# Performance work log

Hardware: AMD Instinct MI355X
Metric: run time of the kernel (lower is better)

Reference implementation:

```python
import jax, jax.numpy as jnp
import numpy as np

B, S, D, H = 2, 2048, 1024, 16
DH = D // H
EPS = 1e-5
LAMBDA_INIT = 0.8


def setup_inputs() -> dict:
    key = jax.random.key(0)
    ks = jax.random.split(key, 16)
    w_std = 1.0 / np.sqrt(D)
    lam_std = LAMBDA_INIT / np.sqrt(DH)
    return {
        "x": jax.random.normal(ks[0], (B, S, D), jnp.float32),
        # Linear weights stored [in, out] (y = x @ W + b), equivalent to torch W.T
        "Wq": jax.random.normal(ks[1], (D, D), jnp.float32) * w_std,
        "bq": jax.random.normal(ks[2], (D,), jnp.float32) * 0.02,
        "Wk": jax.random.normal(ks[3], (D, D), jnp.float32) * w_std,
        "bk": jax.random.normal(ks[4], (D,), jnp.float32) * 0.02,
        "Wv": jax.random.normal(ks[5], (D, D), jnp.float32) * w_std,
        "bv": jax.random.normal(ks[6], (D,), jnp.float32) * 0.02,
        "Wo": jax.random.normal(ks[7], (D, D), jnp.float32) * w_std,
        "bo": jax.random.normal(ks[8], (D,), jnp.float32) * 0.02,
        "lq1": jax.random.normal(ks[9], (H, DH), jnp.float32) * lam_std,
        "lk1": jax.random.normal(ks[10], (H, DH), jnp.float32) * lam_std,
        "lq2": jax.random.normal(ks[11], (H, DH), jnp.float32) * lam_std,
        "lk2": jax.random.normal(ks[12], (H, DH), jnp.float32) * lam_std,
        # per-head GroupNorm(1, head_dim) affine params (torch default init)
        "gn_w": jnp.ones((H, DH), jnp.float32),
        "gn_b": jnp.zeros((H, DH), jnp.float32),
    }


def reference(x, Wq, bq, Wk, bk, Wv, bv, Wo, bo, lq1, lk1, lq2, lk2, gn_w, gn_b):
    b, s, d = x.shape
    h, dh = lq1.shape
    scale = dh ** -0.5

    q = (x @ Wq + bq).reshape(b, s, h, dh)
    k = (x @ Wk + bk).reshape(b, s, h, dh)
    v = (x @ Wv + bv).reshape(b, s, h, dh)

    # differential lambda per head: exp(<lq1,lk1>) - exp(<lq2,lk2>) + lambda_init
    lam = jnp.exp((lq1 * lk1).sum(-1)) - jnp.exp((lq2 * lk2).sum(-1)) + LAMBDA_INIT  # [H]

    scores = jnp.einsum("bihd,bjhd->bhij", q, k) * scale * lam[None, :, None, None]
    attn = jax.nn.softmax(scores, axis=-1)  # no mask in default call path
    out = jnp.einsum("bhij,bjhd->bihd", attn, v)  # [B,S,H,DH]

    # per-head GroupNorm(1, head_dim): normalize over (seq, head_dim) per (batch, head)
    mean = out.mean(axis=(1, 3), keepdims=True)
    var = out.var(axis=(1, 3), keepdims=True)
    normed = (out - mean) * jax.lax.rsqrt(var + EPS)
    normed = normed * gn_w[None, None, :, :] + gn_b[None, None, :, :]

    y = normed.reshape(b, s, d) @ Wo + bo
    return y
```

## Files before the change

### kernel.cpp

```cpp
#include <hip/hip_runtime.h>

#define S_LEN 2048
#define D_DIM 1024
#define H_NUM 16
#define DH 64
#define EPS_GN 1e-5f
#define LAMBDA_INIT 0.8f

typedef unsigned short bfu;
typedef __attribute__((ext_vector_type(8))) short bf16x8;
typedef __attribute__((ext_vector_type(4))) float f32x4;

union FragU { uint4 u; bf16x8 f; };

__device__ inline float bf2f(bfu u){
  union { unsigned int i; float f; } c; c.i = ((unsigned int)u) << 16; return c.f;
}
__device__ inline bfu f2bf(float f){
  union { float f; unsigned int u; } c; c.f = f;
  unsigned int r = c.u + 0x7fffu + ((c.u >> 16) & 1u);
  return (bfu)(r >> 16);
}
__device__ inline unsigned cvtpk(float lo, float hi){
  unsigned r;
  asm("v_cvt_pk_bf16_f32 %0, %1, %2" : "=v"(r) : "v"(lo), "v"(hi));
  return r;
}
__device__ inline void gload16(const void* g, void* lds){
  __builtin_amdgcn_global_load_lds(
      (const __attribute__((address_space(1))) void*)g,
      (__attribute__((address_space(3))) void*)lds, 16, 0, 0);
}
__device__ inline float ldx(const void* p, size_t i, int isf32){
  return isf32 ? ((const float*)p)[i] : bf2f(((const bfu*)p)[i]);
}
__device__ inline float wave_sum(float x){
  #pragma unroll
  for (int off = 32; off; off >>= 1) x += __shfl_xor(x, off, 64);
  return x;
}

__global__ void lambda_kernel(const void* __restrict__ lq1, const void* __restrict__ lk1,
                              const void* __restrict__ lq2, const void* __restrict__ lk2,
                              const unsigned int* __restrict__ gnw_bits,
                              int* __restrict__ flag, float* __restrict__ lam,
                              float* __restrict__ sums){
  const int isf32 = (gnw_bits[0] == 0x3F800000u) ? 1 : 0;
  int t = threadIdx.x;
  if (t == 0) flag[0] = isf32;
  sums[t] = 0.f;
  if (t < H_NUM){
    float s1 = 0.f, s2 = 0.f;
    for (int d = 0; d < DH; ++d){
      s1 += ldx(lq1, t*DH+d, isf32) * ldx(lk1, t*DH+d, isf32);
      s2 += ldx(lq2, t*DH+d, isf32) * ldx(lk2, t*DH+d, isf32);
    }
    lam[t] = expf(s1) - expf(s2) + LAMBDA_INIT;
  }
}

__global__ __launch_bounds__(256) void prep_all(
    const void* __restrict__ x,
    const void* __restrict__ w0, const void* __restrict__ w1,
    const void* __restrict__ w2, const void* __restrict__ w3,
    const int* __restrict__ flag, bfu* __restrict__ xb, bfu* __restrict__ wt)
{
  const int isf32 = flag[0];
  if (blockIdx.x < 2048){
    size_t i = ((size_t)blockIdx.x * 256 + threadIdx.x) * 8;
    if (isf32){
      const float* xf = (const float*)x;
      float4 a = *(const float4*)(xf + i);
      float4 b = *(const float4*)(xf + i + 4);
      bfu o[8] = {f2bf(a.x),f2bf(a.y),f2bf(a.z),f2bf(a.w),f2bf(b.x),f2bf(b.y),f2bf(b.z),f2bf(b.w)};
      *(uint4*)(xb + i) = *(const uint4*)o;
    } else {
      *(uint4*)(xb + i) = *(const uint4*)((const bfu*)x + i);
    }
    return;
  }
  const int widx = blockIdx.x - 2048;
  const int wsel = widx >> 8, tile = widx & 255;
  const void* W = (wsel==0)?w0:(wsel==1)?w1:(wsel==2)?w2:w3;
  bfu* dst = wt + (size_t)wsel * D_DIM * D_DIM;
  __shared__ float Ts[64][65];
  const int r0 = (tile >> 4) * 64, c0 = (tile & 15) * 64;
  const int ty = threadIdx.x >> 6, tx = threadIdx.x & 63;
  #pragma unroll
  for (int rr = 0; rr < 16; ++rr){
    int row = ty*16 + rr;
    Ts[row][tx] = ldx(W, (size_t)(r0 + row) * D_DIM + c0 + tx, isf32);
  }
  __syncthreads();
  #pragma unroll
  for (int rr = 0; rr < 16; ++rr){
    int row = ty*16 + rr;
    dst[(size_t)(c0 + row) * D_DIM + r0 + tx] = f2bf(Ts[tx][row]);
  }
}

__global__ __launch_bounds__(256, 3) void qkv_mfma(
    const bfu* __restrict__ xb, const bfu* __restrict__ wt,
    const void* __restrict__ bq, const void* __restrict__ bk, const void* __restrict__ bv,
    const float* __restrict__ lam, const int* __restrict__ flag,
    bfu* __restrict__ qb, bfu* __restrict__ kb, bfu* __restrict__ vt)
{
  const int isf32 = flag[0];
  const int z = blockIdx.z;
  const bfu* Wt = wt + (size_t)z * D_DIM * D_DIM;
  const void* bias = (z==0)?bq:(z==1)?bk:bv;

  __shared__ __align__(16) ushort As[2][128][32];
  __shared__ __align__(16) ushort Bs[2][128][32];
  const int m0 = blockIdx.x * 128, n0 = blockIdx.y * 128;
  const int t = threadIdx.x, w = t >> 6, lane = t & 63;
  const int quad = lane >> 4, l15 = lane & 15;
  const int mbase = (w >> 1) * 64, nbase = (w & 1) * 64;

  const int srow = w*32 + (lane >> 2);
  const int gchunk = (lane & 3) ^ ((lane >> 3) & 3);
  const size_t aoff = (size_t)(m0 + srow) * D_DIM + gchunk*8;
  const size_t boff = (size_t)(n0 + srow) * D_DIM + gchunk*8;

#define STAGE(buf, k0) {                                                  \
    gload16(xb + aoff + (k0),            &As[buf][w*32][0]);              \
    gload16(xb + aoff + 16*D_DIM + (k0), &As[buf][w*32+16][0]);           \
    gload16(Wt + boff + (k0),            &Bs[buf][w*32][0]);              \
    gload16(Wt + boff + 16*D_DIM + (k0), &Bs[buf][w*32+16][0]);           \
  }

  f32x4 acc[4][4];
  #pragma unroll
  for (int i = 0; i < 4; ++i)
    #pragma unroll
    for (int j = 0; j < 4; ++j){ f32x4 zz = {0.f,0.f,0.f,0.f}; acc[i][j] = zz; }

  const int chq = (quad ^ ((l15 >> 1) & 3)) * 8;

  STAGE(0, 0)
  int buf = 0;
  for (int k0 = 0; k0 < D_DIM; k0 += 32){
    if (k0 + 32 < D_DIM){
      STAGE(buf ^ 1, k0 + 32)
      asm volatile("s_waitcnt vmcnt(4)" ::: "memory");
    } else {
      asm volatile("s_waitcnt vmcnt(0)" ::: "memory");
    }
    __builtin_amdgcn_s_barrier();
    FragU af[4], bf[4];
    #pragma unroll
    for (int mt = 0; mt < 4; ++mt) af[mt].u = *(const uint4*)&As[buf][mbase + mt*16 + l15][chq];
    #pragma unroll
    for (int nt = 0; nt < 4; ++nt) bf[nt].u = *(const uint4*)&Bs[buf][nbase + nt*16 + l15][chq];
    #pragma unroll
    for (int mt = 0; mt < 4; ++mt)
      #pragma unroll
      for (int nt = 0; nt < 4; ++nt)
        acc[mt][nt] = __builtin_amdgcn_mfma_f32_16x16x32_bf16(af[mt].f, bf[nt].f, acc[mt][nt], 0, 0, 0);
    __builtin_amdgcn_s_barrier();
    buf ^= 1;
  }
#undef STAGE

  #pragma unroll
  for (int mt = 0; mt < 4; ++mt){
    const int mrow = m0 + mbase + mt*16 + quad*4;
    #pragma unroll
    for (int nt = 0; nt < 4; ++nt){
      const int n = n0 + nbase + nt*16 + l15;
      const float bn = ldx(bias, n, isf32);
      if (z < 2){
        bfu* out = (z == 0) ? qb : kb;
        const float qs = (z == 0) ? 0.18033688f * lam[n >> 6] : 1.0f;
        #pragma unroll
        for (int r = 0; r < 4; ++r)
          out[(size_t)(mrow + r) * D_DIM + n] = f2bf((acc[mt][nt][r] + bn) * qs);
      } else {
        const int b = mrow >> 11, s = mrow & (S_LEN - 1);
        const int h = n >> 6, d = n & 63;
        ushort4 pk;
        pk.x = f2bf(acc[mt][nt][0] + bn); pk.y = f2bf(acc[mt][nt][1] + bn);
        pk.z = f2bf(acc[mt][nt][2] + bn); pk.w = f2bf(acc[mt][nt][3] + bn);
        *(ushort4*)(vt + (((size_t)(b*H_NUM + h)*DH + d)*S_LEN) + s) = pk;
      }
    }
  }
}

__global__ __launch_bounds__(256) void repack_k(const bfu* __restrict__ kb, bfu* __restrict__ ksw){
  __shared__ __align__(16) ushort L[64][72];
  const int b = blockIdx.z, h = blockIdx.y, j0 = blockIdx.x * 64;
  const int t = threadIdx.x;
  const int bh = b*H_NUM + h;
  {
    const int j = t >> 2, seg = (t & 3) * 16;
    const bfu* src = kb + ((size_t)(b*S_LEN + j0 + j)*H_NUM + h)*DH + seg;
    uint4 a = *(const uint4*)src, c = *(const uint4*)(src + 8);
    *(uint4*)&L[j][seg] = a; *(uint4*)&L[j][seg+8] = c;
  }
  __syncthreads();
  #pragma unroll
  for (int half = 0; half < 2; ++half){
    int c16 = half*256 + t;
    int blk = c16 >> 6;
    int l   = c16 & 63;
    int jt = blk >> 1, c = blk & 1;
    int m = l & 15, q = l >> 4;
    uint4 v = *(const uint4*)&L[jt*16 + m][c*32 + q*8];
    bfu* dst = ksw + (((size_t)bh*128 + (j0>>4) + jt)*2 + c)*512 + (size_t)l*8;
    *(uint4*)dst = v;
  }
}

__global__ __launch_bounds__(256) void repack_v(const bfu* __restrict__ vt, bfu* __restrict__ vsw){
  __shared__ __align__(16) ushort L[64][72];
  const int b = blockIdx.z, h = blockIdx.y, j0 = blockIdx.x * 64;
  const int t = threadIdx.x;
  const int bh = b*H_NUM + h;
  {
    const int d = t >> 2, seg = (t & 3) * 16;
    const bfu* src = vt + ((size_t)bh*DH + d)*S_LEN + j0 + seg;
    uint4 a = *(const uint4*)src, c = *(const uint4*)(src + 8);
    *(uint4*)&L[d][seg] = a; *(uint4*)&L[d][seg+8] = c;
  }
  __syncthreads();
  #pragma unroll
  for (int half = 0; half < 2; ++half){
    int c16 = half*256 + t;
    int blk = c16 >> 6;
    int l   = c16 & 63;
    int dt = blk >> 1, jcl = blk & 1;
    int m = l & 15, q = l >> 4;
    const int jb = jcl*32 + 16*(q>>1) + 4*(q&1);
    uint2 v0 = *(const uint2*)&L[dt*16 + m][jb];
    uint2 v1 = *(const uint2*)&L[dt*16 + m][jb + 8];
    uint4 v; v.x = v0.x; v.y = v0.y; v.z = v1.x; v.w = v1.y;
    bfu* dst = vsw + (((size_t)bh*4 + dt)*64 + (j0>>5) + jcl)*512 + (size_t)l*8;
    *(uint4*)dst = v;
  }
}

__global__ __launch_bounds__(256, 2) void attn_mfma(
    const bfu* __restrict__ qb, const bfu* __restrict__ ksw, const bfu* __restrict__ vsw,
    bfu* __restrict__ o, float* __restrict__ sums)
{
  const int wg = blockIdx.x;
  const int swz = (wg & 7) * 64 + (wg >> 3);
  const int g = swz >> 4;
  const int i0 = (swz & 15) * 128;
  const int h = g & 15, b = g >> 4;
  const int t = threadIdx.x, w = t >> 6, lane = t & 63;
  const int quad = lane >> 4, l15 = lane & 15;
  const int bh = g;

  FragU qf[2][2];
  #pragma unroll
  for (int mt = 0; mt < 2; ++mt){
    const bfu* qrow = qb + ((size_t)(b*S_LEN + i0 + w*32 + mt*16 + l15)*H_NUM + h)*DH;
    qf[mt][0].u = *(const uint4*)(qrow + quad*8);
    qf[mt][1].u = *(const uint4*)(qrow + 32 + quad*8);
  }

  const bfu* kbase = ksw + (size_t)bh*131072 + (size_t)lane*8;
  const bfu* vbase = vsw + (size_t)bh*131072 + (size_t)lane*8;

  f32x4 Oacc[2][4];
  #pragma unroll
  for (int mt = 0; mt < 2; ++mt)
    #pragma unroll
    for (int dt = 0; dt < 4; ++dt){ f32x4 zz = {0.f,0.f,0.f,0.f}; Oacc[mt][dt] = zz; }
  float lsum[2] = {0.f, 0.f};

  FragU kfA[4][2], vfA[2][4], kfB[4][2], vfB[2][4];

#define LOAD_K(KF, J0)                                                          \
  { _Pragma("unroll")                                                           \
    for (int jt = 0; jt < 4; ++jt){                                             \
      const bfu* kr = kbase + (size_t)(((J0)>>4) + jt)*1024;                    \
      KF[jt][0].u = *(const uint4*)kr;                                          \
      KF[jt][1].u = *(const uint4*)(kr + 512);                                  \
    } }
#define LOAD_V(VF, J0)                                                          \
  { _Pragma("unroll")                                                           \
    for (int jt2 = 0; jt2 < 2; ++jt2)                                           \
      _Pragma("unroll")                                                         \
      for (int dt = 0; dt < 4; ++dt)                                            \
        VF[jt2][dt].u = *(const uint4*)(vbase + (size_t)(dt*64 + ((J0)>>5) + jt2)*512); }

#define PROCESS(KF, VF)                                                         \
  {                                                                             \
    f32x4 s[2][4];                                                              \
    __builtin_amdgcn_s_setprio(1);                                              \
    _Pragma("unroll")                                                           \
    for (int jt = 0; jt < 4; ++jt){                                             \
      _Pragma("unroll")                                                         \
      for (int mt = 0; mt < 2; ++mt){                                           \
        f32x4 zz = {0.f,0.f,0.f,0.f};                                           \
        zz = __builtin_amdgcn_mfma_f32_16x16x32_bf16(KF[jt][0].f, qf[mt][0].f, zz, 0, 0, 0); \
        zz = __builtin_amdgcn_mfma_f32_16x16x32_bf16(KF[jt][1].f, qf[mt][1].f, zz, 0, 0, 0); \
        s[mt][jt] = zz;                                                         \
      }                                                                         \
    }                                                                           \
    __builtin_amdgcn_s_setprio(0);                                              \
    _Pragma("unroll")                                                           \
    for (int mt = 0; mt < 2; ++mt){                                             \
      float ps = 0.f;                                                           \
      _Pragma("unroll")                                                         \
      for (int jt = 0; jt < 4; ++jt){                                           \
        _Pragma("unroll")                                                       \
        for (int r = 0; r < 4; ++r){                                            \
          float p = __builtin_exp2f(s[mt][jt][r]);                              \
          s[mt][jt][r] = p;                                                     \
          ps += p;                                                              \
        }                                                                       \
      }                                                                         \
      lsum[mt] += ps;                                                           \
      _Pragma("unroll")                                                         \
      for (int jt2 = 0; jt2 < 2; ++jt2){                                        \
        unsigned pa0 = cvtpk(s[mt][2*jt2][0],   s[mt][2*jt2][1]);               \
        unsigned pa1 = cvtpk(s[mt][2*jt2][2],   s[mt][2*jt2][3]);               \
        unsigned pb0 = cvtpk(s[mt][2*jt2+1][0], s[mt][2*jt2+1][1]);             \
        unsigned pb1 = cvtpk(s[mt][2*jt2+1][2], s[mt][2*jt2+1][3]);             \
        auto r0 = __builtin_amdgcn_permlane32_swap(pa0, pb0, false, false);     \
        auto r1 = __builtin_amdgcn_permlane32_swap(pa1, pb1, false, false);     \
        FragU pf;                                                               \
        pf.u.x = r0[0]; pf.u.y = r1[0]; pf.u.z = r0[1]; pf.u.w = r1[1];         \
        __builtin_amdgcn_s_setprio(1);                                          \
        _Pragma("unroll")                                                       \
        for (int dt = 0; dt < 4; ++dt)                                          \
          Oacc[mt][dt] = __builtin_amdgcn_mfma_f32_16x16x32_bf16(VF[jt2][dt].f, pf.f, Oacc[mt][dt], 0, 0, 0); \
        __builtin_amdgcn_s_setprio(0);                                          \
      }                                                                         \
    }                                                                           \
  }

  LOAD_K(kfA, 0)
  LOAD_V(vfA, 0)
  for (int j0 = 0; j0 < S_LEN; j0 += 128){
    LOAD_K(kfB, j0 + 64)
    LOAD_V(vfB, j0 + 64)
    PROCESS(kfA, vfA)
    if (j0 + 128 < S_LEN){
      LOAD_K(kfA, j0 + 128)
      LOAD_V(vfA, j0 + 128)
    }
    PROCESS(kfB, vfB)
  }
#undef LOAD_K
#undef LOAD_V
#undef PROCESS

  float s1 = 0.f, s2 = 0.f;
  #pragma unroll
  for (int mt = 0; mt < 2; ++mt){
    float l = lsum[mt];
    l += __shfl_xor(l, 16, 64);
    l += __shfl_xor(l, 32, 64);
    float inv = 1.f / l;
    bfu* orow = o + ((size_t)(b*S_LEN + i0 + w*32 + mt*16 + l15)*H_NUM + h)*DH;
    #pragma unroll
    for (int dt = 0; dt < 4; ++dt){
      float v0 = Oacc[mt][dt][0]*inv, v1 = Oacc[mt][dt][1]*inv;
      float v2 = Oacc[mt][dt][2]*inv, v3 = Oacc[mt][dt][3]*inv;
      s1 += (v0+v1) + (v2+v3);
      s2 += (v0*v0+v1*v1) + (v2*v2+v3*v3);
      ushort4 pk;
      pk.x = f2bf(v0); pk.y = f2bf(v1); pk.z = f2bf(v2); pk.w = f2bf(v3);
      *(ushort4*)(orow + dt*16 + quad*4) = pk;
    }
  }
  s1 = wave_sum(s1); s2 = wave_sum(s2);
  __shared__ float r1[4], r2[4];
  if (lane == 0){ r1[w] = s1; r2[w] = s2; }
  __syncthreads();
  if (t == 0){
    atomicAdd(&sums[bh*2+0], r1[0]+r1[1]+r1[2]+r1[3]);
    atomicAdd(&sums[bh*2+1], r2[0]+r2[1]+r2[2]+r2[3]);
  }
}

__global__ __launch_bounds__(256) void gn_fold(
    const bfu* __restrict__ wt,
    const void* __restrict__ bo, const float* __restrict__ sums,
    const void* __restrict__ gnw, const void* __restrict__ gnb,
    const int* __restrict__ flag,
    bfu* __restrict__ wt2, float* __restrict__ beta)
{
  const int isf32 = flag[0];
  const int z = blockIdx.y;
  const int t = threadIdx.x;
  const int n = blockIdx.x*16 + (t >> 4);
  const int seg = t & 15;
  const float invN = 1.f / (float)(S_LEN * DH);
  const float s1 = sums[(z*H_NUM + seg)*2], s2 = sums[(z*H_NUM + seg)*2 + 1];
  const float mu = s1 * invN;
  const float ri = rsqrtf(s2 * invN - mu*mu + EPS_GN);
  const bfu* src = wt + (size_t)n * D_DIM + seg*64;
  bfu* dst = wt2 + (size_t)z * D_DIM * D_DIM + (size_t)n * D_DIM + seg*64;
  float bacc = 0.f;
  #pragma unroll
  for (int i0 = 0; i0 < 64; i0 += 8){
    uint4 wv = *(const uint4*)(src + i0);
    const bfu* wp = (const bfu*)&wv;
    bfu outv[8];
    #pragma unroll
    for (int j = 0; j < 8; ++j){
      const int c = seg*64 + i0 + j;
      const float wq = bf2f(wp[j]);
      const float a = ri * ldx(gnw, c, isf32);
      outv[j] = f2bf(wq * a);
      bacc += (ldx(gnb, c, isf32) - mu * a) * wq;
    }
    *(uint4*)(dst + i0) = *(const uint4*)outv;
  }
  #pragma unroll
  for (int off = 1; off < 16; off <<= 1) bacc += __shfl_xor(bacc, off, 64);
  if (seg == 0) beta[z*D_DIM + n] = bacc + ldx(bo, n, isf32);
}

__global__ __launch_bounds__(256) void oproj_mfma(
    const bfu* __restrict__ ob, const bfu* __restrict__ wt2,
    const float* __restrict__ beta, const int* __restrict__ flag, void* __restrict__ y)
{
  const int isf32 = flag[0];
  __shared__ __align__(16) ushort As[64][40];
  __shared__ __align__(16) ushort Bs[128][40];
  const int m0 = blockIdx.x * 64, n0 = blockIdx.y * 128;
  const int t = threadIdx.x, w = t >> 6, lane = t & 63;
  const int quad = lane >> 4, l15 = lane & 15;
  const int mbase = (w >> 1) * 32, nbase = (w & 1) * 64;
  const int bB = m0 >> 11;
  const bfu* Wt = wt2 + (size_t)bB * D_DIM * D_DIM;
  const float* bet = beta + bB * D_DIM;

  const int arow = t >> 2, aseg = (t & 3) * 8;
  const int brow = t >> 1, bhalf = (t & 1) * 16;

  f32x4 acc[2][4];
  #pragma unroll
  for (int i = 0; i < 2; ++i)
    #pragma unroll
    for (int j = 0; j < 4; ++j){ f32x4 zz = {0.f,0.f,0.f,0.f}; acc[i][j] = zz; }

  for (int k0 = 0; k0 < D_DIM; k0 += 32){
    *(uint4*)&As[arow][aseg] = *(const uint4*)(ob + (size_t)(m0 + arow) * D_DIM + k0 + aseg);
    const bfu* bsrc = Wt + (size_t)(n0 + brow) * D_DIM + k0 + bhalf;
    uint4 b0 = *(const uint4*)bsrc, b1 = *(const uint4*)(bsrc + 8);
    *(uint4*)&Bs[brow][bhalf]     = b0;  *(uint4*)&Bs[brow][bhalf + 8] = b1;
    __syncthreads();
    FragU af[2], bfr[4];
    #pragma unroll
    for (int mt = 0; mt < 2; ++mt) af[mt].u = *(const uint4*)&As[mbase + mt*16 + l15][quad*8];
    #pragma unroll
    for (int nt = 0; nt < 4; ++nt) bfr[nt].u = *(const uint4*)&Bs[nbase + nt*16 + l15][quad*8];
    #pragma unroll
    for (int mt = 0; mt < 2; ++mt)
      #pragma unroll
      for (int nt = 0; nt < 4; ++nt)
        acc[mt][nt] = __builtin_amdgcn_mfma_f32_16x16x32_bf16(af[mt].f, bfr[nt].f, acc[mt][nt], 0, 0, 0);
    __syncthreads();
  }

  #pragma unroll
  for (int mt = 0; mt < 2; ++mt){
    const int mrow = m0 + mbase + mt*16 + quad*4;
    #pragma unroll
    for (int nt = 0; nt < 4; ++nt){
      const int n = n0 + nbase + nt*16 + l15;
      const float bn = bet[n];
      #pragma unroll
      for (int r = 0; r < 4; ++r){
        float val = acc[mt][nt][r] + bn;
        if (isf32) ((float*)y)[(size_t)(mrow + r) * D_DIM + n] = val;
        else       ((bfu*)y)[(size_t)(mrow + r) * D_DIM + n] = f2bf(val);
      }
    }
  }
}

extern "C" void kernel_launch(void* const* d_in, const int* in_sizes, int n_in,
                              void* d_out, int out_size, void* d_ws, size_t ws_size,
                              hipStream_t stream)
{
  const void* x   = d_in[0];
  const void* Wq  = d_in[1];
  const void* bq  = d_in[2];
  const void* Wk  = d_in[3];
  const void* bk  = d_in[4];
  const void* Wv  = d_in[5];
  const void* bv  = d_in[6];
  const void* Wo  = d_in[7];
  const void* bo  = d_in[8];
  const void* lq1 = d_in[9];
  const void* lk1 = d_in[10];
  const void* lq2 = d_in[11];
  const void* lk2 = d_in[12];
  const void* gnw = d_in[13];
  const void* gnb = d_in[14];

  float* ws   = (float*)d_ws;
  int*   flag = (int*)d_ws;
  float* lam  = ws + 16;
  float* sums = ws + 48;

  const size_t MB = 1u << 20;
  char* base = (char*)d_ws + 4096;
  bfu* xb  = (bfu*)(base);
  bfu* wt  = (bfu*)(base + 8*MB);
  bfu* qb  = (bfu*)(base + 16*MB);
  bfu* kb  = (bfu*)(base + 24*MB);
  bfu* vt  = (bfu*)(base + 32*MB);
  bfu* ob  = (bfu*)(base + 40*MB);
  bfu* ksw = xb;
  bfu* vsw = kb;
  bfu* wt2 = vt;
  float* beta = (float*)(base + 36*MB);

  lambda_kernel<<<1, 64, 0, stream>>>(lq1, lk1, lq2, lk2, (const unsigned int*)gnw, flag, lam, sums);
  prep_all<<<3072, 256, 0, stream>>>(x, Wq, Wk, Wv, Wo, flag, xb, wt);
  qkv_mfma<<<dim3(32, 8, 3), 256, 0, stream>>>(xb, wt, bq, bk, bv, lam, flag, qb, kb, vt);
  repack_k<<<dim3(32, 16, 2), 256, 0, stream>>>(kb, ksw);
  repack_v<<<dim3(32, 16, 2), 256, 0, stream>>>(vt, vsw);
  attn_mfma<<<512, 256, 0, stream>>>(qb, ksw, vsw, ob, sums);
  gn_fold<<<dim3(64, 2), 256, 0, stream>>>(wt + (size_t)3*D_DIM*D_DIM, bo, sums, gnw, gnb, flag, wt2, beta);
  oproj_mfma<<<dim3(64, 8), 256, 0, stream>>>(ob, wt2, beta, flag, d_out);
}
```

Before: 262.4 us.

## Stage K/V tiles through double-buffered LDS shared across waves

```diff
diff --git a/kernel.cpp b/kernel.cpp
--- a/kernel.cpp
+++ b/kernel.cpp
@@ -240,10 +240,12 @@
   }
 }
 
-__global__ __launch_bounds__(256, 2) void attn_mfma(
+__global__ __launch_bounds__(256, 3) void attn_mfma(
     const bfu* __restrict__ qb, const bfu* __restrict__ ksw, const bfu* __restrict__ vsw,
     bfu* __restrict__ o, float* __restrict__ sums)
 {
+  __shared__ __align__(16) ushort KV[2][16384];
+
   const int wg = blockIdx.x;
   const int swz = (wg & 7) * 64 + (wg >> 3);
   const int g = swz >> 4;
@@ -261,8 +263,15 @@
     qf[mt][1].u = *(const uint4*)(qrow + 32 + quad*8);
   }
 
-  const bfu* kbase = ksw + (size_t)bh*131072 + (size_t)lane*8;
-  const bfu* vbase = vsw + (size_t)bh*131072 + (size_t)lane*8;
+  const bfu* kg = ksw + (size_t)bh*131072 + (size_t)lane*8;
+  const bfu* vg = vsw + (size_t)bh*131072 + (size_t)lane*8;
+
+#define STAGE(nbuf, tile) {                                                     \
+    gload16(kg + (size_t)((tile)*8 + w)*512,       &KV[nbuf][w*512]);           \
+    gload16(kg + (size_t)((tile)*8 + w + 4)*512,   &KV[nbuf][(w+4)*512]);       \
+    gload16(vg + (size_t)(w*64 + (tile)*2)*512,    &KV[nbuf][8192 + (w*2)*512]);\
+    gload16(vg + (size_t)(w*64 + (tile)*2 + 1)*512,&KV[nbuf][8192 + (w*2+1)*512]);\
+  }
 
   f32x4 Oacc[2][4];
   #pragma unroll
@@ -271,37 +280,32 @@
     for (int dt = 0; dt < 4; ++dt){ f32x4 zz = {0.f,0.f,0.f,0.f}; Oacc[mt][dt] = zz; }
   float lsum[2] = {0.f, 0.f};
 
-  FragU kfA[4][2], vfA[2][4], kfB[4][2], vfB[2][4];
-
-#define LOAD_K(KF, J0)                                                          \
-  { _Pragma("unroll")                                                           \
-    for (int jt = 0; jt < 4; ++jt){                                             \
-      const bfu* kr = kbase + (size_t)(((J0)>>4) + jt)*1024;                    \
-      KF[jt][0].u = *(const uint4*)kr;                                          \
-      KF[jt][1].u = *(const uint4*)(kr + 512);                                  \
-    } }
-#define LOAD_V(VF, J0)                                                          \
-  { _Pragma("unroll")                                                           \
-    for (int jt2 = 0; jt2 < 2; ++jt2)                                           \
-      _Pragma("unroll")                                                         \
-      for (int dt = 0; dt < 4; ++dt)                                            \
-        VF[jt2][dt].u = *(const uint4*)(vbase + (size_t)(dt*64 + ((J0)>>5) + jt2)*512); }
-
-#define PROCESS(KF, VF)                                                         \
+#define PROCESS(CUR)                                                            \
   {                                                                             \
+    const ushort* Kb = &KV[CUR][(size_t)lane*8];                                \
+    const ushort* Vb = &KV[CUR][8192 + (size_t)lane*8];                         \
     f32x4 s[2][4];                                                              \
     __builtin_amdgcn_s_setprio(1);                                              \
     _Pragma("unroll")                                                           \
     for (int jt = 0; jt < 4; ++jt){                                             \
+      FragU k0, k1;                                                             \
+      k0.u = *(const uint4*)&Kb[(jt*2+0)*512];                                  \
+      k1.u = *(const uint4*)&Kb[(jt*2+1)*512];                                  \
       _Pragma("unroll")                                                         \
       for (int mt = 0; mt < 2; ++mt){                                           \
         f32x4 zz = {0.f,0.f,0.f,0.f};                                           \
-        zz = __builtin_amdgcn_mfma_f32_16x16x32_bf16(KF[jt][0].f, qf[mt][0].f, zz, 0, 0, 0); \
-        zz = __builtin_amdgcn_mfma_f32_16x16x32_bf16(KF[jt][1].f, qf[mt][1].f, zz, 0, 0, 0); \
+        zz = __builtin_amdgcn_mfma_f32_16x16x32_bf16(k0.f, qf[mt][0].f, zz, 0, 0, 0); \
+        zz = __builtin_amdgcn_mfma_f32_16x16x32_bf16(k1.f, qf[mt][1].f, zz, 0, 0, 0); \
         s[mt][jt] = zz;                                                         \
       }                                                                         \
     }                                                                           \
     __builtin_amdgcn_s_setprio(0);                                              \
+    FragU vf[2][4];                                                             \
+    _Pragma("unroll")                                                           \
+    for (int jt2 = 0; jt2 < 2; ++jt2)                                           \
+      _Pragma("unroll")                                                         \
+      for (int dt = 0; dt < 4; ++dt)                                            \
+        vf[jt2][dt].u = *(const uint4*)&Vb[(dt*2+jt2)*512];                     \
     _Pragma("unroll")                                                           \
     for (int mt = 0; mt < 2; ++mt){                                             \
       float ps = 0.f;                                                           \
@@ -328,26 +332,28 @@
         __builtin_amdgcn_s_setprio(1);                                          \
         _Pragma("unroll")                                                       \
         for (int dt = 0; dt < 4; ++dt)                                          \
-          Oacc[mt][dt] = __builtin_amdgcn_mfma_f32_16x16x32_bf16(VF[jt2][dt].f, pf.f, Oacc[mt][dt], 0, 0, 0); \
+          Oacc[mt][dt] = __builtin_amdgcn_mfma_f32_16x16x32_bf16(vf[jt2][dt].f, pf.f, Oacc[mt][dt], 0, 0, 0); \
         __builtin_amdgcn_s_setprio(0);                                          \
       }                                                                         \
     }                                                                           \
   }
 
-  LOAD_K(kfA, 0)
-  LOAD_V(vfA, 0)
-  for (int j0 = 0; j0 < S_LEN; j0 += 128){
-    LOAD_K(kfB, j0 + 64)
-    LOAD_V(vfB, j0 + 64)
-    PROCESS(kfA, vfA)
-    if (j0 + 128 < S_LEN){
-      LOAD_K(kfA, j0 + 128)
-      LOAD_V(vfA, j0 + 128)
-    }
-    PROCESS(kfB, vfB)
-  }
-#undef LOAD_K
-#undef LOAD_V
+  STAGE(0, 0)
+  for (int tl = 0; tl < 32; ++tl){
+    const int cur = tl & 1;
+    if (tl + 1 < 32){
+      STAGE(cur ^ 1, tl + 1)
+      asm volatile("s_waitcnt vmcnt(4)" ::: "memory");
+    } else {
+      asm volatile("s_waitcnt vmcnt(0)" ::: "memory");
+    }
+    __builtin_amdgcn_s_barrier();
+    __builtin_amdgcn_sched_barrier(0);
+    PROCESS(cur)
+    __builtin_amdgcn_s_barrier();
+    __builtin_amdgcn_sched_barrier(0);
+  }
+#undef STAGE
 #undef PROCESS
 
   float s1 = 0.f, s2 = 0.f;
```

After: 268.4 us. 2.3% more time.
